# Performance work log

Measured on AMD Instinct MI355X. Metric: run time of the kernel, lower is better.

Reference implementation:

```python
import jax, jax.numpy as jnp
import numpy as np
from jax import lax

GO = 1  # mead-baseline Offsets.GO
NEG = -10000.0


def setup_inputs() -> dict:
    key = jax.random.key(0)
    k1, k2, k3, k4 = jax.random.split(key, 4)
    B, T, K = 1024, 512, 64
    unary = jax.random.normal(k1, (B, T, K), dtype=jnp.float32)
    lengths = jax.random.randint(k2, (B,), 1, T + 1).astype(jnp.int32)
    inv_mask = jax.random.randint(k3, (K, K), 0, 2).astype(jnp.int32)
    A = (jax.random.normal(k4, (K, K), dtype=jnp.float32) * 0.1)
    return {"unary": unary, "lengths": lengths, "inv_mask": inv_mask, "A": A}


def _viterbi(probv, trans, seq_lens):
    """Masked Viterbi decode (tf.contrib.crf.crf_decode semantics).

    probv: [B, T1, K] unary scores (GO frame already prepended)
    trans: [K, K] transition scores, trans[i, j] = score(i -> j)
    seq_lens: [B] int32, valid lengths (already +1 for the GO frame)
    """
    B, T1, K = probv.shape
    alpha0 = probv[:, 0]                      # [B, K]
    us = jnp.swapaxes(probv[:, 1:], 0, 1)     # [T1-1, B, K]
    ts = jnp.arange(1, T1)

    def fwd(alpha, xs):
        u_t, t = xs
        scores = alpha[:, :, None] + trans[None]        # [B, K_prev, K_cur]
        bp = jnp.argmax(scores, axis=1).astype(jnp.int32)  # [B, K]
        new_alpha = jnp.max(scores, axis=1) + u_t
        alpha = jnp.where((t < seq_lens)[:, None], new_alpha, alpha)  # freeze past length
        return alpha, bp

    alpha_f, bps = lax.scan(fwd, alpha0, (us, ts))  # bps: [T1-1, B, K]
    last = jnp.argmax(alpha_f, axis=-1).astype(jnp.int32)  # [B] tag at last valid step
    best = jnp.max(alpha_f, axis=-1)                       # [B]

    def bwd(tag, xs):
        bp_t, t = xs
        prev = jnp.take_along_axis(bp_t, tag[:, None], axis=1)[:, 0]
        prev = jnp.where(t < seq_lens, prev, tag)  # beyond length: carry tag back
        return prev, prev

    _, prevs = lax.scan(bwd, last, (bps[::-1], ts[::-1]))  # prevs: [T1-1, B] (times T1-2..0)
    tags = jnp.concatenate([prevs[::-1], last[None]], axis=0)  # [T1, B]
    return jnp.swapaxes(tags, 0, 1), best


def reference(unary, lengths, inv_mask, A):
    B, T, K = unary.shape
    inv = inv_mask.astype(jnp.float32) * NEG
    trans = jax.nn.log_softmax(A + inv, axis=-1)
    gos = jnp.full((1, 1, K), NEG, dtype=unary.dtype).at[:, :, GO].set(0.0)
    probv = jnp.concatenate([jnp.broadcast_to(gos, (B, 1, K)), unary], axis=1)  # [B, T+1, K]
    viterbi, _ = _viterbi(probv, trans, lengths.astype(jnp.int32) + 1)
    return viterbi[:, 1:]  # drop GO position -> [B, T]
```

## Files before the change

### kernel.cpp

```cpp
#include <hip/hip_runtime.h>

#define NEGV -10000.0f
#define BB 1024
#define TT 512
#define KK 64

typedef float vf2 __attribute__((ext_vector_type(2)));
typedef int   vi2 __attribute__((ext_vector_type(2)));

#define BAR() asm volatile("s_waitcnt lgkmcnt(0)\n\ts_barrier" ::: "memory")

__device__ __forceinline__ float merge_max64(float v)
{
    vi2 r = __builtin_amdgcn_permlane32_swap(__float_as_int(v), __float_as_int(v),
                                             false, false);
    return fmaxf(__int_as_float(r[0]), __int_as_float(r[1]));
}
__device__ __forceinline__ int merge_min64(int v)
{
    vi2 r = __builtin_amdgcn_permlane32_swap(v, v, false, false);
    return min(r[0], r[1]);
}

__global__ __launch_bounds__(64)
void trans_kernel(const float* __restrict__ A, const int* __restrict__ inv,
                  float* __restrict__ trans)
{
    const int i = blockIdx.x, j = threadIdx.x;
    float x = A[i * KK + j] + (inv[i * KK + j] ? NEGV : 0.0f);
    float m = x;
    #pragma unroll
    for (int o = 32; o > 0; o >>= 1) m = fmaxf(m, __shfl_xor(m, o));
    float e = expf(x - m);
    float s = e;
    #pragma unroll
    for (int o = 32; o > 0; o >>= 1) s += __shfl_xor(s, o);
    trans[i * KK + j] = (x - m) - logf(s);
}


__device__ __forceinline__ int imin3(int a, int b, int c) { return min(min(a, b), c); }

#define FILL4(BUF_, RB_)                                                       \
  { _Pragma("unroll")                                                          \
    for (int d_ = 0; d_ < 4; ++d_) {                                           \
        int r_ = (RB_) + d_; if (r_ > TT - 1) r_ = TT - 1;                     \
        BUF_[d_] = ur[r_ * KK + j];                                            \
    } }

#define STEP(T_, UV_, P_)                                                      \
  {                                                                            \
                            \
                      \
    float sv[32];                                                              \
    _Pragma("unroll")                                                          \
    for (int q = 0; q < 8; ++q) {                                              \
        vf2 t01 = vf2{a4[q].x, a4[q].y} + Tr2[2 * q];                          \
        vf2 t23 = vf2{a4[q].z, a4[q].w} + Tr2[2 * q + 1];                      \
        sv[4 * q + 0] = t01.x; sv[4 * q + 1] = t01.y;                          \
        sv[4 * q + 2] = t23.x; sv[4 * q + 3] = t23.y;                          \
    }                                                                          \
                                          \
    float l0[11];                                                              \
    _Pragma("unroll")                                                          \
    for (int i = 0; i < 10; ++i)                                               \
        l0[i] = fmaxf(fmaxf(sv[3 * i], sv[3 * i + 1]), sv[3 * i + 2]);         \
    l0[10] = fmaxf(sv[30], sv[31]);                                            \
    float l1a = fmaxf(fmaxf(l0[0], l0[1]), l0[2]);                             \
    float l1b = fmaxf(fmaxf(l0[3], l0[4]), l0[5]);                             \
    float l1c = fmaxf(fmaxf(l0[6], l0[7]), l0[8]);                             \
    float l1d = fmaxf(l0[9], l0[10]);                                          \
    float mw  = fmaxf(fmaxf(fmaxf(l1a, l1b), l1c), l1d);                       \
    const float m = merge_max64(mw);             \
    float u_ = (UV_);                                                          \
    asm volatile("" : "+v"(u_));                                               \
    if ((T_) <= len) alpha = m + u_;         \
    if (!ishi) sA[P_][j] = alpha;              \
    BAR();                              \
                                  \
                     \
    {                                                                          \
        const float4* p = (const float4*)sA[P_] + (ibase >> 2);                \
        _Pragma("unroll")                                                      \
        for (int q = 0; q < 8; ++q) a4[q] = p[q];                              \
    }                                                                          \
      \
    {                                                                          \
        int c[32];                                                             \
        _Pragma("unroll")                                                      \
        for (int i = 0; i < 32; ++i) c[i] = (sv[i] == m) ? i : 64;             \
        int n0[11];                                                            \
        _Pragma("unroll")                                                      \
        for (int i = 0; i < 10; ++i)                                           \
            n0[i] = imin3(c[3 * i], c[3 * i + 1], c[3 * i + 2]);               \
        n0[10] = min(c[30], c[31]);                                            \
        int n1a = imin3(n0[0], n0[1], n0[2]);                                  \
        int n1b = imin3(n0[3], n0[4], n0[5]);                                  \
        int n1c = imin3(n0[6], n0[7], n0[8]);                                  \
        int n1d = min(n0[9], n0[10]);                                          \
        int cmin = min(min(min(n1a, n1b), n1c), n1d) + ibase;                  \
        int bpi = merge_min64(cmin);                  \
        if (ishi && (T_) >= 2 && (T_) <= len)                                  \
            sbp[((T_) - 2) * KK + j] = (unsigned char)bpi;   \
    }                                                                          \
  }

__global__ __launch_bounds__(128, 2)
void viterbi_kernel(const float* __restrict__ unary, const int* __restrict__ lengths,
                    const float* __restrict__ trans, int* __restrict__ out)
{
    const int tid   = threadIdx.x;
    const int wv    = tid >> 6;
    const int lane  = tid & 63;
    const int sub   = lane & 31;
    const int ibase = (lane >> 5) << 5;
    const bool ishi = (lane >= 32);
    const int j     = wv * 32 + sub;
    const int b     = blockIdx.x;

    __shared__ unsigned char sbp[(TT - 1) * KK];
    __shared__ __align__(16) float sA[2][KK];

    vf2 Tr2[16];
    #pragma unroll
    for (int q = 0; q < 16; ++q) {
        Tr2[q].x = trans[(ibase + 2 * q)     * KK + j];
        Tr2[q].y = trans[(ibase + 2 * q + 1) * KK + j];
    }

    const int len = lengths[b];
    const float* ur = unary + (long)b * (TT * KK);
    int* orow = out + b * TT;

    float ub0[4], ub1[4];
    FILL4(ub0, 0) FILL4(ub1, 4)

    float alpha = (j == 1) ? 0.0f : NEGV;
    if (!ishi) sA[0][j] = alpha;
    BAR();

    float4 a4[8];
    {
        const float4* p = (const float4*)sA[0] + (ibase >> 2);
        #pragma unroll
        for (int q = 0; q < 8; ++q) a4[q] = p[q];
    }

    for (int tb = 1; tb <= len; tb += 8) {
        STEP(tb + 0, ub0[0], 1) STEP(tb + 1, ub0[1], 0)
        STEP(tb + 2, ub0[2], 1) STEP(tb + 3, ub0[3], 0)
        FILL4(ub0, tb + 7)
        STEP(tb + 4, ub1[0], 1) STEP(tb + 5, ub1[1], 0)
        STEP(tb + 6, ub1[2], 1) STEP(tb + 7, ub1[3], 0)
        FILL4(ub1, tb + 11)
    }

    BAR();

    if (wv == 1) return;

    float av = sA[0][lane];
    float mm = av;
    #pragma unroll
    for (int o = 32; o > 0; o >>= 1) mm = fmaxf(mm, __shfl_xor(mm, o));
    unsigned long long msk = __ballot(av == mm);
    int last = __ffsll(msk) - 1;

    for (int jj = len - 1 + lane; jj < TT; jj += 64) orow[jj] = last;

    asm volatile("s_waitcnt lgkmcnt(0)" ::: "memory");

    int tag = last;
    for (int t = len; t >= 2; --t) {
        int prev = sbp[(t - 2) * KK + tag];
        if (lane == 0) orow[t - 2] = prev;
        tag = prev;
    }
}

extern "C" void kernel_launch(void* const* d_in, const int* in_sizes, int n_in,
                              void* d_out, int out_size, void* d_ws, size_t ws_size,
                              hipStream_t stream)
{
    const float* unary   = (const float*)d_in[0];
    const int*   lengths = (const int*)d_in[1];
    const int*   inv     = (const int*)d_in[2];
    const float* A       = (const float*)d_in[3];
    int*         out     = (int*)d_out;

    float* trans = (float*)d_ws;

    trans_kernel<<<KK, KK, 0, stream>>>(A, inv, trans);
    viterbi_kernel<<<BB, 128, 0, stream>>>(unary, lengths, trans, out);
}
```

Before: 426.3 us.

## Store Viterbi backpointers in global memory to shrink LDS footprint

Backpointers now go to a per-batch global workspace buffer instead of a 32 KB LDS array, so each block uses about 8 KB of LDS and more blocks can be resident per CU. The backtrace copies 128-step chunks from global into LDS and walks them there. A fallback kernel that keeps the LDS-only path runs when the workspace is too small. The cost is about 32 MB of extra global writes and reads, plus a vmcnt wait at the barrier.

```diff
diff --git a/kernel.cpp b/kernel.cpp
--- a/kernel.cpp
+++ b/kernel.cpp
@@ -4,6 +4,7 @@
 #define BB 1024
 #define TT 512
 #define KK 64
+#define BPROWS 512
 
 typedef float vf2 __attribute__((ext_vector_type(2)));
 typedef int   vi2 __attribute__((ext_vector_type(2)));
@@ -48,10 +49,12 @@
         BUF_[d_] = ur[r_ * KK + j];                                            \
     } }
 
-#define STEP(T_, UV_, P_)                                                      \
+#define BP_G(t) bpb[((t) - 2) * KK + j] = (unsigned char)bpi
+#define BP_L(t) sbp[((t) - 2) * KK + j] = (unsigned char)bpi
+
+#define STEP(T_, UV_, P_, BPM_)                                                \
   {                                                                            \
                             \
-                      \
     float sv[32];                                                              \
     _Pragma("unroll")                                                          \
     for (int q = 0; q < 8; ++q) {                                              \
@@ -60,7 +63,6 @@
         sv[4 * q + 0] = t01.x; sv[4 * q + 1] = t01.y;                          \
         sv[4 * q + 2] = t23.x; sv[4 * q + 3] = t23.y;                          \
     }                                                                          \
-                                          \
     float l0[11];                                                              \
     _Pragma("unroll")                                                          \
     for (int i = 0; i < 10; ++i)                                               \
@@ -78,13 +80,11 @@
     if (!ishi) sA[P_][j] = alpha;              \
     BAR();                              \
                                   \
-                     \
     {                                                                          \
         const float4* p = (const float4*)sA[P_] + (ibase >> 2);                \
         _Pragma("unroll")                                                      \
         for (int q = 0; q < 8; ++q) a4[q] = p[q];                              \
     }                                                                          \
-      \
     {                                                                          \
         int c[32];                                                             \
         _Pragma("unroll")                                                      \
@@ -100,76 +100,114 @@
         int n1d = min(n0[9], n0[10]);                                          \
         int cmin = min(min(min(n1a, n1b), n1c), n1d) + ibase;                  \
         int bpi = merge_min64(cmin);                  \
-        if (ishi && (T_) >= 2 && (T_) <= len)                                  \
-            sbp[((T_) - 2) * KK + j] = (unsigned char)bpi;   \
+        if (ishi && (T_) >= 2 && (T_) <= len) { BPM_(T_); }                    \
     }                                                                          \
   }
+
+#define VIT_PROLOGUE()                                                         \
+    const int tid   = threadIdx.x;                                             \
+    const int wv    = tid >> 6;                                                \
+    const int lane  = tid & 63;                                                \
+    const int sub   = lane & 31;                                               \
+    const int ibase = (lane >> 5) << 5;                                        \
+    const bool ishi = (lane >= 32);                                            \
+    const int j     = wv * 32 + sub;                                           \
+    const int b     = blockIdx.x;                                              \
+    vf2 Tr2[16];                                                               \
+    _Pragma("unroll")                                                          \
+    for (int q = 0; q < 16; ++q) {                                             \
+        Tr2[q].x = trans[(ibase + 2 * q)     * KK + j];                        \
+        Tr2[q].y = trans[(ibase + 2 * q + 1) * KK + j];                        \
+    }                                                                          \
+    const int len = lengths[b];                                                \
+    const float* ur = unary + (long)b * (TT * KK);                             \
+    int* orow = out + b * TT;                                                  \
+    float ub0[4], ub1[4];                                                      \
+    FILL4(ub0, 0) FILL4(ub1, 4)                                                \
+    float alpha = (j == 1) ? 0.0f : NEGV;                                      \
+    if (!ishi) sA[0][j] = alpha;                                               \
+    BAR();                                                                     \
+    float4 a4[8];                                                              \
+    {                                                                          \
+        const float4* p = (const float4*)sA[0] + (ibase >> 2);                 \
+        _Pragma("unroll")                                                      \
+        for (int q = 0; q < 8; ++q) a4[q] = p[q];                              \
+    }
+
+#define VIT_LOOP(BPM_)                                                         \
+    for (int tb = 1; tb <= len; tb += 8) {                                     \
+        STEP(tb + 0, ub0[0], 1, BPM_) STEP(tb + 1, ub0[1], 0, BPM_)            \
+        STEP(tb + 2, ub0[2], 1, BPM_) STEP(tb + 3, ub0[3], 0, BPM_)            \
+        FILL4(ub0, tb + 7)                                                     \
+        STEP(tb + 4, ub1[0], 1, BPM_) STEP(tb + 5, ub1[1], 0, BPM_)            \
+        STEP(tb + 6, ub1[2], 1, BPM_) STEP(tb + 7, ub1[3], 0, BPM_)            \
+        FILL4(ub1, tb + 11)                                                    \
+    }
+
+#define VIT_LAST()                                                             \
+    float av_ = sA[0][lane];                                                   \
+    float mm = av_;                                                            \
+    _Pragma("unroll")                                                          \
+    for (int o = 32; o > 0; o >>= 1) mm = fmaxf(mm, __shfl_xor(mm, o));        \
+    unsigned long long msk = __ballot(av_ == mm);                              \
+    int last = __ffsll(msk) - 1;                                               \
+    for (int jj = len - 1 + lane; jj < TT; jj += 64) orow[jj] = last;
 
 __global__ __launch_bounds__(128, 2)
 void viterbi_kernel(const float* __restrict__ unary, const int* __restrict__ lengths,
-                    const float* __restrict__ trans, int* __restrict__ out)
-{
-    const int tid   = threadIdx.x;
-    const int wv    = tid >> 6;
-    const int lane  = tid & 63;
-    const int sub   = lane & 31;
-    const int ibase = (lane >> 5) << 5;
-    const bool ishi = (lane >= 32);
-    const int j     = wv * 32 + sub;
-    const int b     = blockIdx.x;
-
+                    const float* __restrict__ trans, unsigned char* __restrict__ bpg,
+                    int* __restrict__ out)
+{
+    __shared__ __align__(16) float sA[2][KK];
+    __shared__ __align__(16) unsigned char chunk[8192];
+
+    VIT_PROLOGUE()
+
+    unsigned char* __restrict__ bpb = bpg + (long)b * (BPROWS * KK);
+
+    VIT_LOOP(BP_G)
+
+    asm volatile("s_waitcnt vmcnt(0) lgkmcnt(0)\n\ts_barrier" ::: "memory");
+    if (wv == 1) return;
+
+    VIT_LAST()
+
+    int tag = last;
+    int t2 = len - 2;
+    while (t2 >= 0) {
+        int base = t2 & ~127;
+        {
+            const int4* src = (const int4*)(bpb + base * KK);
+            int4* dst = (int4*)chunk;
+            #pragma unroll
+            for (int k = 0; k < 8; ++k) dst[lane + 64 * k] = src[lane + 64 * k];
+        }
+        asm volatile("s_waitcnt vmcnt(0) lgkmcnt(0)" ::: "memory");
+        for (; t2 >= base; --t2) {
+            int prev = chunk[(t2 - base) * KK + tag];
+            if (lane == 0) orow[t2] = prev;
+            tag = prev;
+        }
+    }
+}
+
+__global__ __launch_bounds__(128, 2)
+void viterbi_kernel_lds(const float* __restrict__ unary, const int* __restrict__ lengths,
+                        const float* __restrict__ trans, int* __restrict__ out)
+{
     __shared__ unsigned char sbp[(TT - 1) * KK];
     __shared__ __align__(16) float sA[2][KK];
 
-    vf2 Tr2[16];
-    #pragma unroll
-    for (int q = 0; q < 16; ++q) {
-        Tr2[q].x = trans[(ibase + 2 * q)     * KK + j];
-        Tr2[q].y = trans[(ibase + 2 * q + 1) * KK + j];
-    }
-
-    const int len = lengths[b];
-    const float* ur = unary + (long)b * (TT * KK);
-    int* orow = out + b * TT;
-
-    float ub0[4], ub1[4];
-    FILL4(ub0, 0) FILL4(ub1, 4)
-
-    float alpha = (j == 1) ? 0.0f : NEGV;
-    if (!ishi) sA[0][j] = alpha;
+    VIT_PROLOGUE()
+
+    VIT_LOOP(BP_L)
+
     BAR();
-
-    float4 a4[8];
-    {
-        const float4* p = (const float4*)sA[0] + (ibase >> 2);
-        #pragma unroll
-        for (int q = 0; q < 8; ++q) a4[q] = p[q];
-    }
-
-    for (int tb = 1; tb <= len; tb += 8) {
-        STEP(tb + 0, ub0[0], 1) STEP(tb + 1, ub0[1], 0)
-        STEP(tb + 2, ub0[2], 1) STEP(tb + 3, ub0[3], 0)
-        FILL4(ub0, tb + 7)
-        STEP(tb + 4, ub1[0], 1) STEP(tb + 5, ub1[1], 0)
-        STEP(tb + 6, ub1[2], 1) STEP(tb + 7, ub1[3], 0)
-        FILL4(ub1, tb + 11)
-    }
-
-    BAR();
-
     if (wv == 1) return;
 
-    float av = sA[0][lane];
-    float mm = av;
-    #pragma unroll
-    for (int o = 32; o > 0; o >>= 1) mm = fmaxf(mm, __shfl_xor(mm, o));
-    unsigned long long msk = __ballot(av == mm);
-    int last = __ffsll(msk) - 1;
-
-    for (int jj = len - 1 + lane; jj < TT; jj += 64) orow[jj] = last;
+    VIT_LAST()
 
     asm volatile("s_waitcnt lgkmcnt(0)" ::: "memory");
-
     int tag = last;
     for (int t = len; t >= 2; --t) {
         int prev = sbp[(t - 2) * KK + tag];
@@ -189,7 +227,14 @@
     int*         out     = (int*)d_out;
 
     float* trans = (float*)d_ws;
+    unsigned char* bpg = (unsigned char*)d_ws + 16 * 1024;
 
     trans_kernel<<<KK, KK, 0, stream>>>(A, inv, trans);
-    viterbi_kernel<<<BB, 128, 0, stream>>>(unary, lengths, trans, out);
-}
+
+    const size_t need = 16 * 1024 + (size_t)BB * (BPROWS * KK);
+    if (ws_size >= need) {
+        viterbi_kernel<<<BB, 128, 0, stream>>>(unary, lengths, trans, bpg, out);
+    } else {
+        viterbi_kernel_lds<<<BB, 128, 0, stream>>>(unary, lengths, trans, out);
+    }
+}
```

After: 441.9 us. 1.04x slower.
